# Kernel tuning notes

Measured on AMD Instinct MI355X. Metric: run time of the kernel, lower is better.

Reference implementation:

```python
import jax, jax.numpy as jnp
import numpy as np


def setup_inputs() -> dict:
    key = jax.random.key(0)
    k1, k2, k3 = jax.random.split(key, 3)
    B, C, H, W = 4, 3, 1024, 1920
    im0 = jax.random.normal(k1, (B, C, H, W), dtype=jnp.float32)
    # realistic optical-flow displacements of a few pixels
    flow = jax.random.normal(k2, (B, H, W, 2), dtype=jnp.float32) * 5.0
    flowback = jax.random.normal(k3, (B, H, W, 2), dtype=jnp.float32) * 5.0
    return {"im0": im0, "flow": flow, "flowback": flowback, "interpolation_mode": 0}


def _splat(im0, flow, interpolation_mode):
    # im0: [B,C,H,W], flow: [B,H,W,2] (dx, dy)
    B, C, H, W = im0.shape
    src = jnp.transpose(im0, (0, 2, 3, 1)).reshape(B * H * W, C)  # [BHW, C]
    gy, gx = jnp.meshgrid(jnp.arange(H, dtype=jnp.float32),
                          jnp.arange(W, dtype=jnp.float32), indexing="ij")
    x = gx[None] + flow[..., 0]  # [B,H,W] target x coord
    y = gy[None] + flow[..., 1]  # [B,H,W] target y coord
    b_idx = jnp.arange(B, dtype=jnp.int32)[:, None, None] * (H * W)  # batch offset

    out_flat = jnp.zeros((B * H * W, C), dtype=im0.dtype)

    if interpolation_mode == 1:  # Nearest
        xi = jnp.round(x).astype(jnp.int32)
        yi = jnp.round(y).astype(jnp.int32)
        corners = [(xi, yi, jnp.ones_like(x))]
    else:  # Bilinear: scatter-add to 4 neighbors
        x0 = jnp.floor(x).astype(jnp.int32)
        y0 = jnp.floor(y).astype(jnp.int32)
        x1, y1 = x0 + 1, y0 + 1
        x0f, y0f = x0.astype(x.dtype), y0.astype(y.dtype)
        wx1, wy1 = x - x0f, y - y0f
        wx0, wy0 = 1.0 - wx1, 1.0 - wy1
        corners = [(x0, y0, wx0 * wy0), (x1, y0, wx1 * wy0),
                   (x0, y1, wx0 * wy1), (x1, y1, wx1 * wy1)]

    for xi, yi, wgt in corners:
        valid = (xi >= 0) & (xi < W) & (yi >= 0) & (yi < H)
        w = wgt * valid.astype(im0.dtype)
        xc = jnp.clip(xi, 0, W - 1)
        yc = jnp.clip(yi, 0, H - 1)
        idx = (b_idx + yc * W + xc).reshape(-1)  # [BHW]
        out_flat = out_flat.at[idx].add(src * w.reshape(-1, 1))

    return jnp.transpose(out_flat.reshape(B, H, W, C), (0, 3, 1, 2))


def reference(im0, flow, flowback, interpolation_mode):
    # flowback is accepted (as in the CUDA extension signature) but the
    # forward splat itself only consumes im0 and the forward flow.
    return _splat(im0, flow, interpolation_mode)
```

## Files before the change

kernel.cpp:

```cpp
#include <hip/hip_runtime.h>

constexpr int B_ = 4;
constexpr int C_ = 3;
constexpr int H_ = 1024;
constexpr int W_ = 1920;
constexpr int HW_ = H_ * W_;

constexpr int TW = 64;
constexpr int TH = 64;
constexpr int R  = 16;
constexpr int EW = TW + 2 * R;
constexpr int EH = TH + 2 * R;
constexpr int TCELLS = TW * TH;
constexpr int NTHR = 512;
constexpr int QPR = EW / 4;
constexpr int NQ  = QPR * EH;

static_assert(W_ % TW == 0 && H_ % TH == 0, "exact tiling assumed");
static_assert(W_ % 4 == 0 && EW % 4 == 0, "quad alignment assumed");

__global__ __launch_bounds__(NTHR, 6) void fw_gather(
    const float* __restrict__ im0,
    const float2* __restrict__ flow,
    const int* __restrict__ mode_p,
    float* __restrict__ out) {
    __shared__ float tile[C_][TCELLS];

    const int tx0 = blockIdx.x * TW;
    const int ty0 = blockIdx.y * TH;
    const int b   = blockIdx.z;
    const int mode = *mode_p;

    float* t0 = &tile[0][0];
    for (int i = threadIdx.x; i < C_ * TCELLS; i += NTHR) t0[i] = 0.0f;
    __syncthreads();

    const float*  im0b  = im0  + (size_t)b * C_ * HW_;
    const float2* flowb = flow + (size_t)b * HW_;

    for (int q = threadIdx.x; q < NQ; q += NTHR) {
        const int qy = q / QPR;
        const int qx = (q - qy * QPR) * 4;
        const int gy = ty0 - R + qy;
        const int gx = tx0 - R + qx;
        if ((unsigned)gy >= (unsigned)H_) continue;
        if ((unsigned)gx >= (unsigned)W_) continue;

        const int src = gy * W_ + gx;
        const float4 f01 = reinterpret_cast<const float4*>(flowb)[src >> 1];
        const float4 f23 = reinterpret_cast<const float4*>(flowb)[(src >> 1) + 1];
        const float4 sA  = reinterpret_cast<const float4*>(im0b)[src >> 2];
        const float4 sB  = reinterpret_cast<const float4*>(im0b + HW_)[src >> 2];
        const float4 sC  = reinterpret_cast<const float4*>(im0b + 2 * HW_)[src >> 2];

        const float fx[4] = { f01.x, f01.z, f23.x, f23.z };
        const float fy[4] = { f01.y, f01.w, f23.y, f23.w };
        const float s0[4] = { sA.x, sA.y, sA.z, sA.w };
        const float s1[4] = { sB.x, sB.y, sB.z, sB.w };
        const float s2[4] = { sC.x, sC.y, sC.z, sC.w };

        if (mode == 1) {
#pragma unroll
            for (int i = 0; i < 4; ++i) {
                const int gxi = gx + i;
                const int cx = (int)rintf((float)gxi + fx[i]);
                const int cy = (int)rintf((float)gy  + fy[i]);
                const int ltx = cx - tx0, lty = cy - ty0;
                const int dx = cx - gxi, dy = cy - gy;
                if ((unsigned)ltx < (unsigned)TW && (unsigned)lty < (unsigned)TH &&
                    dx >= -R && dx <= R && dy >= -R && dy <= R) {
                    const int idx = lty * TW + ltx;
                    unsafeAtomicAdd(&tile[0][idx], s0[i]);
                    unsafeAtomicAdd(&tile[1][idx], s1[i]);
                    unsafeAtomicAdd(&tile[2][idx], s2[i]);
                }
            }
        } else {
#pragma unroll
            for (int i = 0; i < 4; ++i) {
                const int gxi = gx + i;
                const float px = (float)gxi + fx[i];
                const float py = (float)gy  + fy[i];
                const float xf = floorf(px), yf = floorf(py);
                const int x0 = (int)xf, y0 = (int)yf;
                const float wx1 = px - xf, wy1 = py - yf;
                const float wx0 = 1.0f - wx1, wy0 = 1.0f - wy1;

                const int lx0 = x0 - tx0, ly0 = y0 - ty0;
                const int dx0 = x0 - gxi, dy0 = y0 - gy;
                const bool vx0 = ((unsigned)lx0 < (unsigned)TW) &&
                                 (dx0 >= -R) && (dx0 <= R);
                const bool vx1 = ((unsigned)(lx0 + 1) < (unsigned)TW) &&
                                 (dx0 + 1 >= -R) && (dx0 + 1 <= R);
                const bool vy0 = ((unsigned)ly0 < (unsigned)TH) &&
                                 (dy0 >= -R) && (dy0 <= R);
                const bool vy1 = ((unsigned)(ly0 + 1) < (unsigned)TH) &&
                                 (dy0 + 1 >= -R) && (dy0 + 1 <= R);
                if (!((vx0 || vx1) && (vy0 || vy1))) continue;

                const int idx00 = ly0 * TW + lx0;
                if (vy0) {
                    if (vx0) {
                        const float w = wx0 * wy0;
                        unsafeAtomicAdd(&tile[0][idx00], s0[i] * w);
                        unsafeAtomicAdd(&tile[1][idx00], s1[i] * w);
                        unsafeAtomicAdd(&tile[2][idx00], s2[i] * w);
                    }
                    if (vx1) {
                        const float w = wx1 * wy0;
                        unsafeAtomicAdd(&tile[0][idx00 + 1], s0[i] * w);
                        unsafeAtomicAdd(&tile[1][idx00 + 1], s1[i] * w);
                        unsafeAtomicAdd(&tile[2][idx00 + 1], s2[i] * w);
                    }
                }
                if (vy1) {
                    if (vx0) {
                        const float w = wx0 * wy1;
                        unsafeAtomicAdd(&tile[0][idx00 + TW], s0[i] * w);
                        unsafeAtomicAdd(&tile[1][idx00 + TW], s1[i] * w);
                        unsafeAtomicAdd(&tile[2][idx00 + TW], s2[i] * w);
                    }
                    if (vx1) {
                        const float w = wx1 * wy1;
                        unsafeAtomicAdd(&tile[0][idx00 + TW + 1], s0[i] * w);
                        unsafeAtomicAdd(&tile[1][idx00 + TW + 1], s1[i] * w);
                        unsafeAtomicAdd(&tile[2][idx00 + TW + 1], s2[i] * w);
                    }
                }
            }
        }
    }
    __syncthreads();

    for (int i = threadIdx.x; i < C_ * (TCELLS / 4); i += NTHR) {
        const int c    = i >> 10;
        const int j    = i & 1023;
        const int row  = j >> 4;
        const int col4 = j & 15;
        const float4 v = reinterpret_cast<const float4*>(&tile[c][0])[j];
        float* dst = out + ((size_t)(b * C_ + c)) * HW_ +
                     (size_t)(ty0 + row) * W_ + tx0 + col4 * 4;
        *reinterpret_cast<float4*>(dst) = v;
    }
}

__global__ __launch_bounds__(256) void fw_far(
    const float* __restrict__ im0,
    const float2* __restrict__ flow,
    const int* __restrict__ mode_p,
    float* __restrict__ out) {
    const int idx = blockIdx.x * 256 + threadIdx.x;
    if (idx >= B_ * HW_) return;

    const float2 f = flow[idx];
    const float lim = (float)(R - 1);
    if (fabsf(f.x) < lim && fabsf(f.y) < lim) return;

    const int mode = *mode_p;
    const int b   = idx / HW_;
    const int rem = idx - b * HW_;
    const int gy  = rem / W_;
    const int gx  = rem - gy * W_;
    const float px = (float)gx + f.x;
    const float py = (float)gy + f.y;
    const float* im0b = im0 + (size_t)b * C_ * HW_;
    float*       outb = out + (size_t)b * C_ * HW_;
    const int src = gy * W_ + gx;

    if (mode == 1) {
        const int cx = (int)rintf(px);
        const int cy = (int)rintf(py);
        const int dx = cx - gx, dy = cy - gy;
        const bool in = (unsigned)cx < (unsigned)W_ &&
                        (unsigned)cy < (unsigned)H_;
        if (in && (dx < -R || dx > R || dy < -R || dy > R)) {
            const int dsti = cy * W_ + cx;
            unsafeAtomicAdd(outb + dsti,            im0b[src]);
            unsafeAtomicAdd(outb + HW_ + dsti,      im0b[src + HW_]);
            unsafeAtomicAdd(outb + 2 * HW_ + dsti,  im0b[src + 2 * HW_]);
        }
    } else {
        const float xf = floorf(px), yf = floorf(py);
        const int x0 = (int)xf, y0 = (int)yf;
        const float wx1 = px - xf, wy1 = py - yf;
        const float wx0 = 1.0f - wx1, wy0 = 1.0f - wy1;

        const int   cxs[4] = { x0, x0 + 1, x0,     x0 + 1 };
        const int   cys[4] = { y0, y0,     y0 + 1, y0 + 1 };
        const float cws[4] = { wx0 * wy0, wx1 * wy0, wx0 * wy1, wx1 * wy1 };

        bool m[4];
        bool any = false;
#pragma unroll
        for (int k = 0; k < 4; ++k) {
            const int dx = cxs[k] - gx, dy = cys[k] - gy;
            const bool in = (unsigned)cxs[k] < (unsigned)W_ &&
                            (unsigned)cys[k] < (unsigned)H_;
            m[k] = in && (dx < -R || dx > R || dy < -R || dy > R);
            any = any || m[k];
        }
        if (!any) return;

        const float s0 = im0b[src];
        const float s1 = im0b[src + HW_];
        const float s2 = im0b[src + 2 * HW_];
#pragma unroll
        for (int k = 0; k < 4; ++k) {
            if (m[k]) {
                const int dsti = cys[k] * W_ + cxs[k];
                const float w = cws[k];
                unsafeAtomicAdd(outb + dsti,           s0 * w);
                unsafeAtomicAdd(outb + HW_ + dsti,     s1 * w);
                unsafeAtomicAdd(outb + 2 * HW_ + dsti, s2 * w);
            }
        }
    }
}

extern "C" void kernel_launch(void* const* d_in, const int* in_sizes, int n_in,
                              void* d_out, int out_size, void* d_ws, size_t ws_size,
                              hipStream_t stream) {
    const float*  im0  = (const float*)d_in[0];
    const float2* flow = (const float2*)d_in[1];
    const int*    mode = (const int*)d_in[3];
    float* out = (float*)d_out;

    dim3 grid(W_ / TW, H_ / TH, B_);
    fw_gather<<<grid, dim3(NTHR), 0, stream>>>(im0, flow, mode, out);

    constexpr int total = B_ * HW_;
    fw_far<<<dim3((total + 255) / 256), dim3(256), 0, stream>>>(im0, flow, mode, out);
}
```

Baseline: 694.8 us.

## Record far-displacement pixels during gather and process only the compacted list

The tiled gather kernel now spots core pixels whose flow reaches beyond the halo radius. It appends their linear indices to a workspace list through a global atomic counter. A small grid-stride kernel then scatters only those listed pixels, replacing the full-image pass that re-read the whole flow field. Each shared-memory channel plane is also padded by four floats. The costs are an extra memset launch and global atomic traffic on one counter, and the path depends on workspace size: if the workspace is too small it falls back to the old full scan.

After: 724.8 us. 1.04x slower.

```diff
diff --git a/kernel.cpp b/kernel.cpp
--- a/kernel.cpp
+++ b/kernel.cpp
@@ -12,6 +12,7 @@
 constexpr int EW = TW + 2 * R;
 constexpr int EH = TH + 2 * R;
 constexpr int TCELLS = TW * TH;
+constexpr int PLANE  = TCELLS + 4;
 constexpr int NTHR = 512;
 constexpr int QPR = EW / 4;
 constexpr int NQ  = QPR * EH;
@@ -23,16 +24,18 @@
     const float* __restrict__ im0,
     const float2* __restrict__ flow,
     const int* __restrict__ mode_p,
-    float* __restrict__ out) {
-    __shared__ float tile[C_][TCELLS];
+    float* __restrict__ out,
+    int* __restrict__ far_cnt,
+    int* __restrict__ far_rec,
+    const int far_cap) {
+    __shared__ float tile[C_ * PLANE];
 
     const int tx0 = blockIdx.x * TW;
     const int ty0 = blockIdx.y * TH;
     const int b   = blockIdx.z;
     const int mode = *mode_p;
 
-    float* t0 = &tile[0][0];
-    for (int i = threadIdx.x; i < C_ * TCELLS; i += NTHR) t0[i] = 0.0f;
+    for (int i = threadIdx.x; i < C_ * PLANE; i += NTHR) tile[i] = 0.0f;
     __syncthreads();
 
     const float*  im0b  = im0  + (size_t)b * C_ * HW_;
@@ -40,11 +43,13 @@
 
     for (int q = threadIdx.x; q < NQ; q += NTHR) {
         const int qy = q / QPR;
-        const int qx = (q - qy * QPR) * 4;
+        const int qxl = (q - qy * QPR) * 4;
         const int gy = ty0 - R + qy;
-        const int gx = tx0 - R + qx;
+        const int gx = tx0 - R + qxl;
         if ((unsigned)gy >= (unsigned)H_) continue;
         if ((unsigned)gx >= (unsigned)W_) continue;
+        const bool is_core = ((unsigned)(qy - R) < (unsigned)TH) &&
+                             ((unsigned)(qxl - R) < (unsigned)TW);
 
         const int src = gy * W_ + gx;
         const float4 f01 = reinterpret_cast<const float4*>(flowb)[src >> 1];
@@ -58,6 +63,18 @@
         const float s0[4] = { sA.x, sA.y, sA.z, sA.w };
         const float s1[4] = { sB.x, sB.y, sB.z, sB.w };
         const float s2[4] = { sC.x, sC.y, sC.z, sC.w };
+
+        if (far_cap > 0 && is_core) {
+            const float lim = (float)(R - 1);
+#pragma unroll
+            for (int i = 0; i < 4; ++i) {
+                if (!(fabsf(fx[i]) < lim && fabsf(fy[i]) < lim)) {
+                    const int slot = atomicAdd(far_cnt, 1);
+                    if (slot < far_cap)
+                        far_rec[slot] = b * HW_ + gy * W_ + (gx + i);
+                }
+            }
+        }
 
         if (mode == 1) {
 #pragma unroll
@@ -70,9 +87,9 @@
                 if ((unsigned)ltx < (unsigned)TW && (unsigned)lty < (unsigned)TH &&
                     dx >= -R && dx <= R && dy >= -R && dy <= R) {
                     const int idx = lty * TW + ltx;
-                    unsafeAtomicAdd(&tile[0][idx], s0[i]);
-                    unsafeAtomicAdd(&tile[1][idx], s1[i]);
-                    unsafeAtomicAdd(&tile[2][idx], s2[i]);
+                    unsafeAtomicAdd(&tile[0 * PLANE + idx], s0[i]);
+                    unsafeAtomicAdd(&tile[1 * PLANE + idx], s1[i]);
+                    unsafeAtomicAdd(&tile[2 * PLANE + idx], s2[i]);
                 }
             }
         } else {
@@ -102,29 +119,29 @@
                 if (vy0) {
                     if (vx0) {
                         const float w = wx0 * wy0;
-                        unsafeAtomicAdd(&tile[0][idx00], s0[i] * w);
-                        unsafeAtomicAdd(&tile[1][idx00], s1[i] * w);
-                        unsafeAtomicAdd(&tile[2][idx00], s2[i] * w);
+                        unsafeAtomicAdd(&tile[0 * PLANE + idx00], s0[i] * w);
+                        unsafeAtomicAdd(&tile[1 * PLANE + idx00], s1[i] * w);
+                        unsafeAtomicAdd(&tile[2 * PLANE + idx00], s2[i] * w);
                     }
                     if (vx1) {
                         const float w = wx1 * wy0;
-                        unsafeAtomicAdd(&tile[0][idx00 + 1], s0[i] * w);
-                        unsafeAtomicAdd(&tile[1][idx00 + 1], s1[i] * w);
-                        unsafeAtomicAdd(&tile[2][idx00 + 1], s2[i] * w);
+                        unsafeAtomicAdd(&tile[0 * PLANE + idx00 + 1], s0[i] * w);
+                        unsafeAtomicAdd(&tile[1 * PLANE + idx00 + 1], s1[i] * w);
+                        unsafeAtomicAdd(&tile[2 * PLANE + idx00 + 1], s2[i] * w);
                     }
                 }
                 if (vy1) {
                     if (vx0) {
                         const float w = wx0 * wy1;
-                        unsafeAtomicAdd(&tile[0][idx00 + TW], s0[i] * w);
-                        unsafeAtomicAdd(&tile[1][idx00 + TW], s1[i] * w);
-                        unsafeAtomicAdd(&tile[2][idx00 + TW], s2[i] * w);
+                        unsafeAtomicAdd(&tile[0 * PLANE + idx00 + TW], s0[i] * w);
+                        unsafeAtomicAdd(&tile[1 * PLANE + idx00 + TW], s1[i] * w);
+                        unsafeAtomicAdd(&tile[2 * PLANE + idx00 + TW], s2[i] * w);
                     }
                     if (vx1) {
                         const float w = wx1 * wy1;
-                        unsafeAtomicAdd(&tile[0][idx00 + TW + 1], s0[i] * w);
-                        unsafeAtomicAdd(&tile[1][idx00 + TW + 1], s1[i] * w);
-                        unsafeAtomicAdd(&tile[2][idx00 + TW + 1], s2[i] * w);
+                        unsafeAtomicAdd(&tile[0 * PLANE + idx00 + TW + 1], s0[i] * w);
+                        unsafeAtomicAdd(&tile[1 * PLANE + idx00 + TW + 1], s1[i] * w);
+                        unsafeAtomicAdd(&tile[2 * PLANE + idx00 + TW + 1], s2[i] * w);
                     }
                 }
             }
@@ -137,32 +154,19 @@
         const int j    = i & 1023;
         const int row  = j >> 4;
         const int col4 = j & 15;
-        const float4 v = reinterpret_cast<const float4*>(&tile[c][0])[j];
+        const float4 v =
+            *reinterpret_cast<const float4*>(&tile[c * PLANE + (j << 2)]);
         float* dst = out + ((size_t)(b * C_ + c)) * HW_ +
                      (size_t)(ty0 + row) * W_ + tx0 + col4 * 4;
         *reinterpret_cast<float4*>(dst) = v;
     }
 }
 
-__global__ __launch_bounds__(256) void fw_far(
-    const float* __restrict__ im0,
-    const float2* __restrict__ flow,
-    const int* __restrict__ mode_p,
-    float* __restrict__ out) {
-    const int idx = blockIdx.x * 256 + threadIdx.x;
-    if (idx >= B_ * HW_) return;
-
-    const float2 f = flow[idx];
-    const float lim = (float)(R - 1);
-    if (fabsf(f.x) < lim && fabsf(f.y) < lim) return;
-
-    const int mode = *mode_p;
-    const int b   = idx / HW_;
-    const int rem = idx - b * HW_;
-    const int gy  = rem / W_;
-    const int gx  = rem - gy * W_;
-    const float px = (float)gx + f.x;
-    const float py = (float)gy + f.y;
+__device__ __forceinline__ void far_pixel_body(
+    const float* __restrict__ im0, float* __restrict__ out,
+    int b, int gx, int gy, float fxv, float fyv, int mode) {
+    const float px = (float)gx + fxv;
+    const float py = (float)gy + fyv;
     const float* im0b = im0 + (size_t)b * C_ * HW_;
     float*       outb = out + (size_t)b * C_ * HW_;
     const int src = gy * W_ + gx;
@@ -217,6 +221,46 @@
     }
 }
 
+__global__ __launch_bounds__(256) void fw_far_rec(
+    const float* __restrict__ im0,
+    const float2* __restrict__ flow,
+    const int* __restrict__ mode_p,
+    float* __restrict__ out,
+    const int* __restrict__ far_cnt,
+    const int* __restrict__ far_rec,
+    const int far_cap) {
+    const int mode = *mode_p;
+    int n = *far_cnt;
+    if (n > far_cap) n = far_cap;
+    for (int i = blockIdx.x * 256 + threadIdx.x; i < n; i += gridDim.x * 256) {
+        const int pix = far_rec[i];
+        const int b   = pix / HW_;
+        const int rem = pix - b * HW_;
+        const int gy  = rem / W_;
+        const int gx  = rem - gy * W_;
+        const float2 f = flow[pix];
+        far_pixel_body(im0, out, b, gx, gy, f.x, f.y, mode);
+    }
+}
+
+__global__ __launch_bounds__(256) void fw_far_scan(
+    const float* __restrict__ im0,
+    const float2* __restrict__ flow,
+    const int* __restrict__ mode_p,
+    float* __restrict__ out) {
+    const int idx = blockIdx.x * 256 + threadIdx.x;
+    if (idx >= B_ * HW_) return;
+    const float2 f = flow[idx];
+    const float lim = (float)(R - 1);
+    if (fabsf(f.x) < lim && fabsf(f.y) < lim) return;
+    const int mode = *mode_p;
+    const int b   = idx / HW_;
+    const int rem = idx - b * HW_;
+    const int gy  = rem / W_;
+    const int gx  = rem - gy * W_;
+    far_pixel_body(im0, out, b, gx, gy, f.x, f.y, mode);
+}
+
 extern "C" void kernel_launch(void* const* d_in, const int* in_sizes, int n_in,
                               void* d_out, int out_size, void* d_ws, size_t ws_size,
                               hipStream_t stream) {
@@ -226,8 +270,25 @@
     float* out = (float*)d_out;
 
     dim3 grid(W_ / TW, H_ / TH, B_);
-    fw_gather<<<grid, dim3(NTHR), 0, stream>>>(im0, flow, mode, out);
-
-    constexpr int total = B_ * HW_;
-    fw_far<<<dim3((total + 255) / 256), dim3(256), 0, stream>>>(im0, flow, mode, out);
-}
+
+    int* cnt = (int*)d_ws;
+    int* rec = cnt + 16;
+    const long long cap_ll = (long long)(ws_size / 4) - 16;
+    const int cap = (ws_size >= (1u << 16))
+                        ? (int)(cap_ll > 0x7fffffff ? 0x7fffffff : cap_ll)
+                        : 0;
+
+    if (cap > 0) {
+        (void)hipMemsetAsync(d_ws, 0, sizeof(int), stream);
+        fw_gather<<<grid, dim3(NTHR), 0, stream>>>(im0, flow, mode, out,
+                                                   cnt, rec, cap);
+        fw_far_rec<<<dim3(256), dim3(256), 0, stream>>>(im0, flow, mode, out,
+                                                        cnt, rec, cap);
+    } else {
+        fw_gather<<<grid, dim3(NTHR), 0, stream>>>(im0, flow, mode, out,
+                                                   nullptr, nullptr, 0);
+        constexpr int total = B_ * HW_;
+        fw_far_scan<<<dim3((total + 255) / 256), dim3(256), 0, stream>>>(
+            im0, flow, mode, out);
+    }
+}
```
